# Kernel optimization log

Hardware: AMD Instinct MI355X
Metric: run time of the kernel (lower is better)

Reference implementation:

```python
import jax, jax.numpy as jnp
import numpy as np

N_HEADS = 4
TAU = 0.1

def _ln(x, w, b):
    m = jnp.mean(x, axis=-1, keepdims=True)
    v = jnp.mean(jnp.square(x - m), axis=-1, keepdims=True)
    return (x - m) / jnp.sqrt(v + 1e-6) * w + b

def _l2norm(x):
    # torch F.normalize(dim=1): x / max(||x||_2, 1e-12)
    n = jnp.linalg.norm(x, axis=1, keepdims=True)
    return x / jnp.maximum(n, 1e-12)

def _sincos_pe(T, dim):
    pos = jnp.arange(T, dtype=jnp.float32)[:, None]
    div = jnp.exp(jnp.arange(0, dim, 2, dtype=jnp.float32) * (-np.log(10000.0) / dim))
    ang = pos * div[None, :]
    # interleave: even indices sin, odd indices cos
    return jnp.stack([jnp.sin(ang), jnp.cos(ang)], axis=-1).reshape(T, dim)

def reference(x, p1_w, p1_b, pln1_w, pln1_b, p2_w, pln2_w, pln2_b,
              in_proj_w, in_proj_b, out_proj_w, out_proj_b,
              ln1_w, ln1_b, lin1_w, lin1_b, lin2_w, lin2_b, ln2_w, ln2_b, head_w):
    B, T, D = x.shape
    E = p2_w.shape[0]           # bottleneck_dim = 256
    H = N_HEADS
    hd = E // H
    # projector: Linear -> LN -> GELU -> Linear(no bias) -> LN
    h = jax.nn.gelu(_ln(x.reshape(B * T, D) @ p1_w.T + p1_b, pln1_w, pln1_b), approximate=False)
    h = _ln(h @ p2_w.T, pln2_w, pln2_b).reshape(B, T, E)
    h = h + _sincos_pe(T, E)[None]
    causal = jnp.tril(jnp.ones((T, T), dtype=bool))
    L = in_proj_w.shape[0]
    for i in range(L):  # post-norm TransformerEncoderLayer
        qkv = h @ in_proj_w[i].T + in_proj_b[i]        # [B,T,3E]
        q, k, v = jnp.split(qkv, 3, axis=-1)
        q = q.reshape(B, T, H, hd).transpose(0, 2, 1, 3)
        k = k.reshape(B, T, H, hd).transpose(0, 2, 1, 3)
        v = v.reshape(B, T, H, hd).transpose(0, 2, 1, 3)
        scores = jnp.einsum('bhtd,bhsd->bhts', q, k) / np.float32(np.sqrt(hd))
        scores = jnp.where(causal[None, None], scores, -jnp.inf)
        probs = jax.nn.softmax(scores, axis=-1)        # materialized attn probs (eager path)
        attn = jnp.einsum('bhts,bhsd->bhtd', probs, v).transpose(0, 2, 1, 3).reshape(B, T, E)
        attn = attn @ out_proj_w[i].T + out_proj_b[i]
        h = _ln(h + attn, ln1_w[i], ln1_b[i])
        ff = jax.nn.gelu(h @ lin1_w[i].T + lin1_b[i], approximate=False) @ lin2_w[i].T + lin2_b[i]
        h = _ln(h + ff, ln2_w[i], ln2_b[i])
    flat = _l2norm(h.reshape(B * T, E))
    wn = _l2norm(head_w)
    return (flat @ wn.T / TAU).reshape(B, T, -1)

def setup_inputs() -> dict:
    key = jax.random.key(0)
    ks = jax.random.split(key, 8)
    B, T, D, E, HID, CLS, L = 2048, 20, 2048, 256, 1024, 1000, 2
    s = 0.02
    def w(k, shape):
        return jax.random.normal(k, shape, jnp.float32) * s
    return {
        'x': jax.random.normal(ks[0], (B, T, D), jnp.float32),
        'p1_w': w(ks[1], (HID, D)), 'p1_b': jnp.zeros((HID,), jnp.float32),
        'pln1_w': jnp.ones((HID,), jnp.float32), 'pln1_b': jnp.zeros((HID,), jnp.float32),
        'p2_w': w(ks[2], (E, HID)),
        'pln2_w': jnp.ones((E,), jnp.float32), 'pln2_b': jnp.zeros((E,), jnp.float32),
        'in_proj_w': w(ks[3], (L, 3 * E, E)), 'in_proj_b': jnp.zeros((L, 3 * E), jnp.float32),
        'out_proj_w': w(ks[4], (L, E, E)), 'out_proj_b': jnp.zeros((L, E), jnp.float32),
        'ln1_w': jnp.ones((L, E), jnp.float32), 'ln1_b': jnp.zeros((L, E), jnp.float32),
        'lin1_w': w(ks[5], (L, 4 * E, E)), 'lin1_b': jnp.zeros((L, 4 * E), jnp.float32),
        'lin2_w': w(ks[6], (L, E, 4 * E)), 'lin2_b': jnp.zeros((L, E), jnp.float32),
        'ln2_w': jnp.ones((L, E), jnp.float32), 'ln2_b': jnp.zeros((L, E), jnp.float32),
        'head_w': w(ks[7], (CLS, E)),
    }
```

## Files before the change

kernel.cpp:

```cpp
#include <hip/hip_runtime.h>
#include <math.h>

#define CDIV(a,b) (((a)+(b)-1)/(b))

typedef unsigned short bfu;
typedef short   s16x8 __attribute__((ext_vector_type(8)));
typedef float   f32x4 __attribute__((ext_vector_type(4)));

#define GLOAD16(gp, lp) __builtin_amdgcn_global_load_lds( \
    (const __attribute__((address_space(1))) void*)(gp),  \
    (__attribute__((address_space(3))) void*)(lp), 16, 0, 0)

static __device__ __forceinline__ float gelu_exact(float x) {
    return 0.5f * x * (1.0f + erff(x * 0.7071067811865475f));
}
static __device__ __forceinline__ bfu f2bf(float x) {
    unsigned int u = __float_as_uint(x);
    unsigned int r = u + 0x7fffu + ((u >> 16) & 1u);
    return (bfu)(r >> 16);
}
static __device__ __forceinline__ float bf2f(bfu b) {
    return __uint_as_float(((unsigned int)b) << 16);
}

static __device__ __forceinline__ float block_sum_256(float v, float* sbuf) {
    #pragma unroll
    for (int off = 32; off; off >>= 1) v += __shfl_down(v, off, 64);
    const int lane = threadIdx.x & 63;
    const int wid  = threadIdx.x >> 6;
    __syncthreads();
    if (lane == 0) sbuf[wid] = v;
    __syncthreads();
    return sbuf[0] + sbuf[1] + sbuf[2] + sbuf[3];
}

__global__ __launch_bounds__(256)
void cvt_kernel(const float* __restrict__ in, bfu* __restrict__ out, int n4)
{
    int i = blockIdx.x * 256 + threadIdx.x;
    const int stride = gridDim.x * 256;
    for (; i < n4; i += stride) {
        float4 f = ((const float4*)in)[i];
        ushort4 o;
        o.x = f2bf(f.x); o.y = f2bf(f.y); o.z = f2bf(f.z); o.w = f2bf(f.w);
        ((ushort4*)out)[i] = o;
    }
}

__global__ __launch_bounds__(256)
void cvt6_kernel(const float* __restrict__ s0, const float* __restrict__ s1,
                 const float* __restrict__ s2, const float* __restrict__ s3,
                 const float* __restrict__ s4, const float* __restrict__ s5,
                 bfu* __restrict__ dst)
{
    const int c0 = 524288;
    const int c1 = c0 + 65536;
    const int c2 = c1 + 98304;
    const int c3 = c2 + 32768;
    const int c4 = c3 + 131072;
    const int c5 = c4 + 131072;
    int i = blockIdx.x * 256 + threadIdx.x;
    const int stride = gridDim.x * 256;
    for (; i < c5; i += stride) {
        const float* s; int base;
        if      (i < c0) { s = s0; base = 0;  }
        else if (i < c1) { s = s1; base = c0; }
        else if (i < c2) { s = s2; base = c1; }
        else if (i < c3) { s = s3; base = c2; }
        else if (i < c4) { s = s4; base = c3; }
        else             { s = s5; base = c4; }
        float4 f = ((const float4*)s)[i - base];
        ushort4 o;
        o.x = f2bf(f.x); o.y = f2bf(f.y); o.z = f2bf(f.z); o.w = f2bf(f.w);
        ((ushort4*)dst)[i] = o;
    }
}

template<bool GELU_EP, bool OUT_BF16>
__global__ __launch_bounds__(256)
void mfma_gemm(const bfu* __restrict__ A, const bfu* __restrict__ W,
               const float* __restrict__ bias, void* __restrict__ Cv,
               int M, int N, int K, float scale, int ntx)
{
    __shared__ bfu As[128 * 32];
    __shared__ bfu Ws[128 * 32];

    const int tid = threadIdx.x;
    const int nwg = gridDim.x;
    const int lid = (nwg & 7) ? (int)blockIdx.x
                              : ((int)blockIdx.x & 7) * (nwg >> 3) + ((int)blockIdx.x >> 3);
    const int row0 = (lid / ntx) * 128;
    const int col0 = (lid % ntx) * 128;

    const int lane = tid & 63;
    const int wave = tid >> 6;
    const int wm = (wave >> 1) * 64;
    const int wn = (wave & 1) * 64;
    const int fr = lane & 15;
    const int fk = (lane >> 4) * 8;

    const int lrow = lane >> 2;
    const int lk   = (lane & 3) * 8;
    const bfu* al0 = A + (size_t)(row0 + wave * 32 + lrow) * K + lk;
    const bfu* al1 = al0 + (size_t)16 * K;
    const bfu* wl0 = W + (size_t)(col0 + wave * 32 + lrow) * K + lk;
    const bfu* wl1 = wl0 + (size_t)16 * K;
    bfu* ad0 = &As[(wave * 2    ) * 512];
    bfu* ad1 = &As[(wave * 2 + 1) * 512];
    bfu* wd0 = &Ws[(wave * 2    ) * 512];
    bfu* wd1 = &Ws[(wave * 2 + 1) * 512];

    f32x4 acc[4][4];
    #pragma unroll
    for (int i = 0; i < 4; ++i)
        #pragma unroll
        for (int j = 0; j < 4; ++j) acc[i][j] = (f32x4)0.f;

    for (int k0 = 0; k0 < K; k0 += 32) {
        GLOAD16(al0 + k0, ad0);
        GLOAD16(al1 + k0, ad1);
        GLOAD16(wl0 + k0, wd0);
        GLOAD16(wl1 + k0, wd1);
        __syncthreads();

        s16x8 af[4], wf[4];
        #pragma unroll
        for (int i = 0; i < 4; ++i) af[i] = *(const s16x8*)&As[(wm + 16*i + fr) * 32 + fk];
        #pragma unroll
        for (int j = 0; j < 4; ++j) wf[j] = *(const s16x8*)&Ws[(wn + 16*j + fr) * 32 + fk];

        #pragma unroll
        for (int i = 0; i < 4; ++i)
            #pragma unroll
            for (int j = 0; j < 4; ++j)
                acc[i][j] = __builtin_amdgcn_mfma_f32_16x16x32_bf16(af[i], wf[j], acc[i][j], 0, 0, 0);
        __syncthreads();
    }

    #pragma unroll
    for (int i = 0; i < 4; ++i) {
        const int r = row0 + wm + 16 * i + (lane >> 4) * 4;
        #pragma unroll
        for (int j = 0; j < 4; ++j) {
            const int c = col0 + wn + 16 * j + fr;
            if (c < N) {
                const float bsum = bias ? bias[c] : 0.f;
                #pragma unroll
                for (int rr = 0; rr < 4; ++rr) {
                    float v = acc[i][j][rr] + bsum;
                    if (GELU_EP) v = gelu_exact(v);
                    v *= scale;
                    if (OUT_BF16) ((bfu*)Cv)[(size_t)(r + rr) * N + c] = f2bf(v);
                    else          ((float*)Cv)[(size_t)(r + rr) * N + c] = v;
                }
            }
        }
    }
}

template<int VPT, bool GELU_EP, bool ADD_PE, bool RES, bool IN_BF16>
__global__ __launch_bounds__(256)
void ln_kernel(const void* __restrict__ Xv, const float* __restrict__ R,
               const float* __restrict__ w, const float* __restrict__ b,
               float* __restrict__ Yf, bfu* __restrict__ Yb, int T)
{
    const int W = VPT * 256;
    __shared__ float sbuf[4];
    const int row = blockIdx.x;

    float v[VPT];
    if (IN_BF16) {
        const bfu* xr = (const bfu*)Xv + (size_t)row * W;
        if (VPT == 4) {
            ushort4 t4 = *(const ushort4*)(xr + threadIdx.x * 4);
            v[0] = bf2f(t4.x); v[1] = bf2f(t4.y); v[2] = bf2f(t4.z); v[3] = bf2f(t4.w);
        } else {
            v[0] = bf2f(xr[threadIdx.x]);
        }
    } else {
        const float* xr = (const float*)Xv + (size_t)row * W;
        if (VPT == 4) {
            float4 t4 = *(const float4*)(xr + threadIdx.x * 4);
            v[0] = t4.x; v[1] = t4.y; v[2] = t4.z; v[3] = t4.w;
        } else {
            v[0] = xr[threadIdx.x];
        }
    }
    if (RES) {
        #pragma unroll
        for (int j = 0; j < VPT; ++j)
            v[j] += R[(size_t)row * W + ((VPT == 4) ? threadIdx.x * 4 + j : (int)threadIdx.x)];
    }

    float s = 0.f;
    #pragma unroll
    for (int j = 0; j < VPT; ++j) s += v[j];
    const float mean = block_sum_256(s, sbuf) / (float)W;

    float q = 0.f;
    #pragma unroll
    for (int j = 0; j < VPT; ++j) { float d = v[j] - mean; q += d * d; }
    const float var  = block_sum_256(q, sbuf) / (float)W;
    const float rstd = rsqrtf(var + 1e-6f);

    #pragma unroll
    for (int j = 0; j < VPT; ++j) {
        const int c = (VPT == 4) ? (threadIdx.x * 4 + j) : (int)threadIdx.x;
        float y = (v[j] - mean) * rstd * w[c] + b[c];
        if (GELU_EP) y = gelu_exact(y);
        if (ADD_PE) {
            const int t = row % T;
            const float cc  = (float)(c & ~1);
            const float div = expf(cc * (-9.210340371976184f / 256.0f));
            const float ang = (float)t * div;
            y += (c & 1) ? cosf(ang) : sinf(ang);
        }
        if (Yf) Yf[(size_t)row * W + c] = y;
        if (Yb) Yb[(size_t)row * W + c] = f2bf(y);
    }
}

__global__ __launch_bounds__(64)
void attn_kernel(const bfu* __restrict__ qkv, bfu* __restrict__ out,
                 int B, int T, int H)
{
    __shared__ float qs[20][65];
    __shared__ float ks[20][65];
    __shared__ float vs[20][65];
    __shared__ float probs[64];

    const int blk = blockIdx.x;
    const int b = blk / H;
    const int h = blk % H;
    const int tid = threadIdx.x;

    for (int t = 0; t < T; ++t) {
        const bfu* base = qkv + (size_t)(b * T + t) * 768 + h * 64 + tid;
        qs[t][tid] = bf2f(base[0]);
        ks[t][tid] = bf2f(base[256]);
        vs[t][tid] = bf2f(base[512]);
    }
    __syncthreads();

    for (int t = 0; t < T; ++t) {
        float sc = -INFINITY;
        if (tid <= t) {
            float s = 0.f;
            #pragma unroll
            for (int d = 0; d < 64; ++d) s = fmaf(qs[t][d], ks[tid][d], s);
            sc = s * 0.125f;
        }
        float m = sc;
        #pragma unroll
        for (int off = 32; off; off >>= 1) m = fmaxf(m, __shfl_xor(m, off, 64));
        float p = (tid <= t) ? expf(sc - m) : 0.f;
        float sum = p;
        #pragma unroll
        for (int off = 32; off; off >>= 1) sum += __shfl_xor(sum, off, 64);
        p /= sum;
        probs[tid] = p;
        __syncthreads();

        float o = 0.f;
        for (int s = 0; s <= t; ++s) o = fmaf(probs[s], vs[s][tid], o);
        out[(size_t)(b * T + t) * 256 + h * 64 + tid] = f2bf(o);
        __syncthreads();
    }
}

__global__ __launch_bounds__(256)
void l2norm_kernel(const float* __restrict__ X, bfu* __restrict__ Y)
{
    __shared__ float sbuf[4];
    const int row = blockIdx.x;
    const float v = X[(size_t)row * 256 + threadIdx.x];
    float s = v * v;
    #pragma unroll
    for (int off = 32; off; off >>= 1) s += __shfl_down(s, off, 64);
    const int lane = threadIdx.x & 63, wid = threadIdx.x >> 6;
    if (lane == 0) sbuf[wid] = s;
    __syncthreads();
    float n = sqrtf(sbuf[0] + sbuf[1] + sbuf[2] + sbuf[3]);
    n = fmaxf(n, 1e-12f);
    Y[(size_t)row * 256 + threadIdx.x] = f2bf(v / n);
}

extern "C" void kernel_launch(void* const* d_in, const int* in_sizes, int n_in,
                              void* d_out, int out_size, void* d_ws, size_t ws_size,
                              hipStream_t stream)
{
    const float* x         = (const float*)d_in[0];
    const float* p1_w      = (const float*)d_in[1];
    const float* p1_b      = (const float*)d_in[2];
    const float* pln1_w    = (const float*)d_in[3];
    const float* pln1_b    = (const float*)d_in[4];
    const float* p2_w      = (const float*)d_in[5];
    const float* pln2_w    = (const float*)d_in[6];
    const float* pln2_b    = (const float*)d_in[7];
    const float* in_proj_w = (const float*)d_in[8];
    const float* in_proj_b = (const float*)d_in[9];
    const float* out_proj_w= (const float*)d_in[10];
    const float* out_proj_b= (const float*)d_in[11];
    const float* ln1_w     = (const float*)d_in[12];
    const float* ln1_b     = (const float*)d_in[13];
    const float* lin1_w    = (const float*)d_in[14];
    const float* lin1_b    = (const float*)d_in[15];
    const float* lin2_w    = (const float*)d_in[16];
    const float* lin2_b    = (const float*)d_in[17];
    const float* ln2_w     = (const float*)d_in[18];
    const float* ln2_b     = (const float*)d_in[19];
    const float* head_w    = (const float*)d_in[20];

    const int B = 2048, T = 20, E = 256, HID = 1024, CLS = 1000, L = 2, H = 4;
    const int M = B * T;
    const int D = 2048;

    char* p = (char*)d_ws;
    bfu*   xb     = (bfu*)p;    p += (size_t)M * D * 2;
    bfu*   h1b    = (bfu*)p;    p += (size_t)M * HID * 2;
    bfu*   wblk   = (bfu*)p;    p += (size_t)3932160 * 2;
    bfu*   wnb    = (bfu*)p;    p += (size_t)1024 * E * 2;

    char* q = (char*)xb;
    float* h      = (float*)q;  q += (size_t)M * E * 4;
    float* ffout  = (float*)q;  q += (size_t)M * E * 4;
    bfu*   hb     = (bfu*)q;    q += (size_t)M * E * 2;
    bfu*   abf    = (bfu*)q;    q += (size_t)M * E * 2;

    bfu* p1wb  = wblk;
    bfu* p2wb  = p1wb  + (size_t)HID * D;
    bfu* qkvwb = p2wb  + (size_t)E * HID;
    bfu* outwb = qkvwb + (size_t)L * 3 * E * E;
    bfu* l1wb  = outwb + (size_t)L * E * E;
    bfu* l2wb  = l1wb  + (size_t)L * 4 * E * E;

    float* out   = (float*)d_out;
    bfu*   qkvb  = (bfu*)d_out;
    float* attnp = (float*)d_out;

    cvt_kernel<<<2048, 256, 0, stream>>>(x, xb, M * D / 4);
    cvt6_kernel<<<2048, 256, 0, stream>>>(p1_w, p2_w, in_proj_w, out_proj_w, lin1_w, lin2_w, wblk);

    mfma_gemm<false, true><<<dim3(8 * (M/128)), 256, 0, stream>>>(
        xb, p1wb, p1_b, h1b, M, HID, D, 1.f, 8);
    ln_kernel<4, true, false, false, true><<<M, 256, 0, stream>>>(
        h1b, nullptr, pln1_w, pln1_b, nullptr, h1b, T);
    mfma_gemm<false, false><<<dim3(2 * (M/128)), 256, 0, stream>>>(
        h1b, p2wb, nullptr, h, M, E, HID, 1.f, 2);
    ln_kernel<1, false, true, false, false><<<M, 256, 0, stream>>>(
        h, nullptr, pln2_w, pln2_b, h, hb, T);

    for (int l = 0; l < L; ++l) {
        mfma_gemm<false, true><<<dim3(6 * (M/128)), 256, 0, stream>>>(
            hb, qkvwb + (size_t)l * 3*E*E, in_proj_b + (size_t)l * 3*E, qkvb, M, 3*E, E, 1.f, 6);
        attn_kernel<<<B * H, 64, 0, stream>>>(qkvb, abf, B, T, H);
        mfma_gemm<false, false><<<dim3(2 * (M/128)), 256, 0, stream>>>(
            abf, outwb + (size_t)l * E*E, out_proj_b + (size_t)l * E, attnp, M, E, E, 1.f, 2);
        ln_kernel<1, false, false, true, false><<<M, 256, 0, stream>>>(
            h, attnp, ln1_w + (size_t)l * E, ln1_b + (size_t)l * E, h, hb, T);
        mfma_gemm<true, true><<<dim3(8 * (M/128)), 256, 0, stream>>>(
            hb, l1wb + (size_t)l * 4*E*E, lin1_b + (size_t)l * 4*E, h1b, M, HID, E, 1.f, 8);
        mfma_gemm<false, false><<<dim3(2 * (M/128)), 256, 0, stream>>>(
            h1b, l2wb + (size_t)l * E*4*E, lin2_b + (size_t)l * E, ffout, M, E, HID, 1.f, 2);
        ln_kernel<1, false, false, true, false><<<M, 256, 0, stream>>>(
            h, ffout, ln2_w + (size_t)l * E, ln2_b + (size_t)l * E, h, hb, T);
    }

    l2norm_kernel<<<M, 256, 0, stream>>>(h, hb);
    l2norm_kernel<<<CLS, 256, 0, stream>>>(head_w, wnb);
    mfma_gemm<false, false><<<dim3(8 * (M/128)), 256, 0, stream>>>(
        hb, wnb, nullptr, out, M, CLS, E, 10.f, 8);
}
```

Measured before the change: 1.391 ms.

## Double-buffer GEMM LDS with XOR swizzle; wave-per-row LayerNorm and precomputed PE

The GEMM now double-buffers its LDS tiles. It prefetches the next K-slice with global_load_lds while running MFMAs on the current one, applies an XOR swizzle to cut LDS bank conflicts, and raises wave priority around the MFMA block. The 256-wide LayerNorm and L2-norm kernels now map one row per wave with float4 loads and shuffle-only reductions, which removes block-level syncs. A 1024-wide LN variant is specialised. The positional encoding is computed once into a small table instead of per element with transcendentals. Trade-offs are twice the LDS use, which may lower occupancy, and one extra tiny launch.

```diff
diff --git a/kernel.cpp b/kernel.cpp
--- a/kernel.cpp
+++ b/kernel.cpp
@@ -22,16 +22,10 @@
 static __device__ __forceinline__ float bf2f(bfu b) {
     return __uint_as_float(((unsigned int)b) << 16);
 }
-
-static __device__ __forceinline__ float block_sum_256(float v, float* sbuf) {
+static __device__ __forceinline__ float wave_sum(float v) {
     #pragma unroll
-    for (int off = 32; off; off >>= 1) v += __shfl_down(v, off, 64);
-    const int lane = threadIdx.x & 63;
-    const int wid  = threadIdx.x >> 6;
-    __syncthreads();
-    if (lane == 0) sbuf[wid] = v;
-    __syncthreads();
-    return sbuf[0] + sbuf[1] + sbuf[2] + sbuf[3];
+    for (int off = 32; off; off >>= 1) v += __shfl_xor(v, off, 64);
+    return v;
 }
 
 __global__ __launch_bounds__(256)
@@ -76,14 +70,24 @@
     }
 }
 
+__global__ __launch_bounds__(256)
+void pe_kernel(float* __restrict__ pe)
+{
+    const int t = blockIdx.x;
+    const int c = threadIdx.x;
+    const float div = expf((float)(c & ~1) * (-9.210340371976184f / 256.0f));
+    const float ang = (float)t * div;
+    pe[t * 256 + c] = (c & 1) ? cosf(ang) : sinf(ang);
+}
+
 template<bool GELU_EP, bool OUT_BF16>
 __global__ __launch_bounds__(256)
 void mfma_gemm(const bfu* __restrict__ A, const bfu* __restrict__ W,
                const float* __restrict__ bias, void* __restrict__ Cv,
                int M, int N, int K, float scale, int ntx)
 {
-    __shared__ bfu As[128 * 32];
-    __shared__ bfu Ws[128 * 32];
+    __shared__ bfu As[2][128 * 32];
+    __shared__ bfu Ws[2][128 * 32];
 
     const int tid = threadIdx.x;
     const int nwg = gridDim.x;
@@ -97,18 +101,16 @@
     const int wm = (wave >> 1) * 64;
     const int wn = (wave & 1) * 64;
     const int fr = lane & 15;
-    const int fk = (lane >> 4) * 8;
+    const int fs = (((lane >> 4) ^ (fr & 3))) * 8;
 
     const int lrow = lane >> 2;
-    const int lk   = (lane & 3) * 8;
+    const int lk   = (((lane & 3) ^ (lrow & 3))) * 8;
     const bfu* al0 = A + (size_t)(row0 + wave * 32 + lrow) * K + lk;
     const bfu* al1 = al0 + (size_t)16 * K;
     const bfu* wl0 = W + (size_t)(col0 + wave * 32 + lrow) * K + lk;
     const bfu* wl1 = wl0 + (size_t)16 * K;
-    bfu* ad0 = &As[(wave * 2    ) * 512];
-    bfu* ad1 = &As[(wave * 2 + 1) * 512];
-    bfu* wd0 = &Ws[(wave * 2    ) * 512];
-    bfu* wd1 = &Ws[(wave * 2 + 1) * 512];
+    const int ld0 = (wave * 2    ) * 512;
+    const int ld1 = (wave * 2 + 1) * 512;
 
     f32x4 acc[4][4];
     #pragma unroll
@@ -116,25 +118,42 @@
         #pragma unroll
         for (int j = 0; j < 4; ++j) acc[i][j] = (f32x4)0.f;
 
+    GLOAD16(al0, &As[0][ld0]);
+    GLOAD16(al1, &As[0][ld1]);
+    GLOAD16(wl0, &Ws[0][ld0]);
+    GLOAD16(wl1, &Ws[0][ld1]);
+    asm volatile("s_waitcnt vmcnt(0)" ::: "memory");
+    __builtin_amdgcn_s_barrier();
+
+    int cur = 0;
     for (int k0 = 0; k0 < K; k0 += 32) {
-        GLOAD16(al0 + k0, ad0);
-        GLOAD16(al1 + k0, ad1);
-        GLOAD16(wl0 + k0, wd0);
-        GLOAD16(wl1 + k0, wd1);
-        __syncthreads();
+        const bool more = (k0 + 32) < K;
+        if (more) {
+            GLOAD16(al0 + k0 + 32, &As[cur ^ 1][ld0]);
+            GLOAD16(al1 + k0 + 32, &As[cur ^ 1][ld1]);
+            GLOAD16(wl0 + k0 + 32, &Ws[cur ^ 1][ld0]);
+            GLOAD16(wl1 + k0 + 32, &Ws[cur ^ 1][ld1]);
+        }
 
         s16x8 af[4], wf[4];
         #pragma unroll
-        for (int i = 0; i < 4; ++i) af[i] = *(const s16x8*)&As[(wm + 16*i + fr) * 32 + fk];
-        #pragma unroll
-        for (int j = 0; j < 4; ++j) wf[j] = *(const s16x8*)&Ws[(wn + 16*j + fr) * 32 + fk];
-
+        for (int i = 0; i < 4; ++i) af[i] = *(const s16x8*)&As[cur][(wm + 16*i + fr) * 32 + fs];
+        #pragma unroll
+        for (int j = 0; j < 4; ++j) wf[j] = *(const s16x8*)&Ws[cur][(wn + 16*j + fr) * 32 + fs];
+
+        __builtin_amdgcn_s_setprio(1);
         #pragma unroll
         for (int i = 0; i < 4; ++i)
             #pragma unroll
             for (int j = 0; j < 4; ++j)
                 acc[i][j] = __builtin_amdgcn_mfma_f32_16x16x32_bf16(af[i], wf[j], acc[i][j], 0, 0, 0);
-        __syncthreads();
+        __builtin_amdgcn_s_setprio(0);
+
+        if (more) {
+            asm volatile("s_waitcnt vmcnt(0)" ::: "memory");
+            __builtin_amdgcn_s_barrier();
+        }
+        cur ^= 1;
     }
 
     #pragma unroll
@@ -158,65 +177,78 @@
     }
 }
 
-template<int VPT, bool GELU_EP, bool ADD_PE, bool RES, bool IN_BF16>
-__global__ __launch_bounds__(256)
-void ln_kernel(const void* __restrict__ Xv, const float* __restrict__ R,
-               const float* __restrict__ w, const float* __restrict__ b,
-               float* __restrict__ Yf, bfu* __restrict__ Yb, int T)
-{
-    const int W = VPT * 256;
+__global__ __launch_bounds__(256)
+void ln1024_kernel(const bfu* __restrict__ X, const float* __restrict__ w,
+                   const float* __restrict__ b, bfu* __restrict__ Y)
+{
     __shared__ float sbuf[4];
     const int row = blockIdx.x;
-
-    float v[VPT];
-    if (IN_BF16) {
-        const bfu* xr = (const bfu*)Xv + (size_t)row * W;
-        if (VPT == 4) {
-            ushort4 t4 = *(const ushort4*)(xr + threadIdx.x * 4);
-            v[0] = bf2f(t4.x); v[1] = bf2f(t4.y); v[2] = bf2f(t4.z); v[3] = bf2f(t4.w);
-        } else {
-            v[0] = bf2f(xr[threadIdx.x]);
-        }
-    } else {
-        const float* xr = (const float*)Xv + (size_t)row * W;
-        if (VPT == 4) {
-            float4 t4 = *(const float4*)(xr + threadIdx.x * 4);
-            v[0] = t4.x; v[1] = t4.y; v[2] = t4.z; v[3] = t4.w;
-        } else {
-            v[0] = xr[threadIdx.x];
-        }
-    }
-    if (RES) {
-        #pragma unroll
-        for (int j = 0; j < VPT; ++j)
-            v[j] += R[(size_t)row * W + ((VPT == 4) ? threadIdx.x * 4 + j : (int)threadIdx.x)];
-    }
-
-    float s = 0.f;
-    #pragma unroll
-    for (int j = 0; j < VPT; ++j) s += v[j];
-    const float mean = block_sum_256(s, sbuf) / (float)W;
+    const bfu* xr = X + (size_t)row * 1024;
+
+    ushort4 t4 = *(const ushort4*)(xr + threadIdx.x * 4);
+    float v[4] = {bf2f(t4.x), bf2f(t4.y), bf2f(t4.z), bf2f(t4.w)};
+
+    float s = v[0] + v[1] + v[2] + v[3];
+    s = wave_sum(s);
+    const int lane = threadIdx.x & 63, wid = threadIdx.x >> 6;
+    if (lane == 0) sbuf[wid] = s;
+    __syncthreads();
+    const float mean = (sbuf[0] + sbuf[1] + sbuf[2] + sbuf[3]) * (1.f / 1024.f);
 
     float q = 0.f;
     #pragma unroll
-    for (int j = 0; j < VPT; ++j) { float d = v[j] - mean; q += d * d; }
-    const float var  = block_sum_256(q, sbuf) / (float)W;
+    for (int j = 0; j < 4; ++j) { float d = v[j] - mean; q += d * d; }
+    q = wave_sum(q);
+    __syncthreads();
+    if (lane == 0) sbuf[wid] = q;
+    __syncthreads();
+    const float var  = (sbuf[0] + sbuf[1] + sbuf[2] + sbuf[3]) * (1.f / 1024.f);
     const float rstd = rsqrtf(var + 1e-6f);
 
+    ushort4 o;
     #pragma unroll
-    for (int j = 0; j < VPT; ++j) {
-        const int c = (VPT == 4) ? (threadIdx.x * 4 + j) : (int)threadIdx.x;
-        float y = (v[j] - mean) * rstd * w[c] + b[c];
-        if (GELU_EP) y = gelu_exact(y);
-        if (ADD_PE) {
-            const int t = row % T;
-            const float cc  = (float)(c & ~1);
-            const float div = expf(cc * (-9.210340371976184f / 256.0f));
-            const float ang = (float)t * div;
-            y += (c & 1) ? cosf(ang) : sinf(ang);
-        }
-        if (Yf) Yf[(size_t)row * W + c] = y;
-        if (Yb) Yb[(size_t)row * W + c] = f2bf(y);
+    for (int j = 0; j < 4; ++j) {
+        const int c = threadIdx.x * 4 + j;
+        float y = gelu_exact((v[j] - mean) * rstd * w[c] + b[c]);
+        ((bfu*)&o)[j] = f2bf(y);
+    }
+    *(ushort4*)(Y + (size_t)row * 1024 + threadIdx.x * 4) = o;
+}
+
+template<bool ADD_PE, bool RES>
+__global__ __launch_bounds__(256)
+void ln256_kernel(const float* __restrict__ X, const float* __restrict__ R,
+                  const float* __restrict__ w, const float* __restrict__ b,
+                  const float* __restrict__ pe, float* __restrict__ Yf,
+                  bfu* __restrict__ Yb, int T)
+{
+    const int row  = blockIdx.x * 4 + (threadIdx.x >> 6);
+    const int lane = threadIdx.x & 63;
+
+    float4 v = *(const float4*)(X + (size_t)row * 256 + lane * 4);
+    if (RES) {
+        float4 r4 = *(const float4*)(R + (size_t)row * 256 + lane * 4);
+        v.x += r4.x; v.y += r4.y; v.z += r4.z; v.w += r4.w;
+    }
+
+    const float mean = wave_sum(v.x + v.y + v.z + v.w) * (1.f / 256.f);
+    float q = (v.x-mean)*(v.x-mean) + (v.y-mean)*(v.y-mean)
+            + (v.z-mean)*(v.z-mean) + (v.w-mean)*(v.w-mean);
+    const float rstd = rsqrtf(wave_sum(q) * (1.f / 256.f) + 1e-6f);
+
+    const float4 w4 = *(const float4*)(w + lane * 4);
+    const float4 b4 = *(const float4*)(b + lane * 4);
+    float y[4] = {(v.x-mean)*rstd*w4.x + b4.x, (v.y-mean)*rstd*w4.y + b4.y,
+                  (v.z-mean)*rstd*w4.z + b4.z, (v.w-mean)*rstd*w4.w + b4.w};
+    if (ADD_PE) {
+        const float4 p4 = *(const float4*)(pe + (size_t)(row % T) * 256 + lane * 4);
+        y[0] += p4.x; y[1] += p4.y; y[2] += p4.z; y[3] += p4.w;
+    }
+
+    if (Yf) *(float4*)(Yf + (size_t)row * 256 + lane * 4) = float4{y[0], y[1], y[2], y[3]};
+    if (Yb) {
+        ushort4 o = {f2bf(y[0]), f2bf(y[1]), f2bf(y[2]), f2bf(y[3])};
+        *(ushort4*)(Yb + (size_t)row * 256 + lane * 4) = o;
     }
 }
 
@@ -271,18 +303,13 @@
 __global__ __launch_bounds__(256)
 void l2norm_kernel(const float* __restrict__ X, bfu* __restrict__ Y)
 {
-    __shared__ float sbuf[4];
-    const int row = blockIdx.x;
-    const float v = X[(size_t)row * 256 + threadIdx.x];
-    float s = v * v;
-    #pragma unroll
-    for (int off = 32; off; off >>= 1) s += __shfl_down(s, off, 64);
-    const int lane = threadIdx.x & 63, wid = threadIdx.x >> 6;
-    if (lane == 0) sbuf[wid] = s;
-    __syncthreads();
-    float n = sqrtf(sbuf[0] + sbuf[1] + sbuf[2] + sbuf[3]);
-    n = fmaxf(n, 1e-12f);
-    Y[(size_t)row * 256 + threadIdx.x] = f2bf(v / n);
+    const int row  = blockIdx.x * 4 + (threadIdx.x >> 6);
+    const int lane = threadIdx.x & 63;
+    float4 v = *(const float4*)(X + (size_t)row * 256 + lane * 4);
+    float n = sqrtf(wave_sum(v.x*v.x + v.y*v.y + v.z*v.z + v.w*v.w));
+    n = 1.f / fmaxf(n, 1e-12f);
+    ushort4 o = {f2bf(v.x*n), f2bf(v.y*n), f2bf(v.z*n), f2bf(v.w*n)};
+    *(ushort4*)(Y + (size_t)row * 256 + lane * 4) = o;
 }
 
 extern "C" void kernel_launch(void* const* d_in, const int* in_sizes, int n_in,
@@ -320,6 +347,7 @@
     bfu*   h1b    = (bfu*)p;    p += (size_t)M * HID * 2;
     bfu*   wblk   = (bfu*)p;    p += (size_t)3932160 * 2;
     bfu*   wnb    = (bfu*)p;    p += (size_t)1024 * E * 2;
+    float* pe     = (float*)p;  p += (size_t)T * 256 * 4;
 
     char* q = (char*)xb;
     float* h      = (float*)q;  q += (size_t)M * E * 4;
@@ -340,15 +368,15 @@
 
     cvt_kernel<<<2048, 256, 0, stream>>>(x, xb, M * D / 4);
     cvt6_kernel<<<2048, 256, 0, stream>>>(p1_w, p2_w, in_proj_w, out_proj_w, lin1_w, lin2_w, wblk);
+    pe_kernel<<<T, 256, 0, stream>>>(pe);
 
     mfma_gemm<false, true><<<dim3(8 * (M/128)), 256, 0, stream>>>(
         xb, p1wb, p1_b, h1b, M, HID, D, 1.f, 8);
-    ln_kernel<4, true, false, false, true><<<M, 256, 0, stream>>>(
-        h1b, nullptr, pln1_w, pln1_b, nullptr, h1b, T);
+    ln1024_kernel<<<M, 256, 0, stream>>>(h1b, pln1_w, pln1_b, h1b);
     mfma_gemm<false, false><<<dim3(2 * (M/128)), 256, 0, stream>>>(
         h1b, p2wb, nullptr, h, M, E, HID, 1.f, 2);
-    ln_kernel<1, false, true, false, false><<<M, 256, 0, stream>>>(
-        h, nullptr, pln2_w, pln2_b, h, hb, T);
+    ln256_kernel<true, false><<<M/4, 256, 0, stream>>>(
+        h, nullptr, pln2_w, pln2_b, pe, h, hb, T);
 
     for (int l = 0; l < L; ++l) {
         mfma_gemm<false, true><<<dim3(6 * (M/128)), 256, 0, stream>>>(
@@ -356,18 +384,18 @@
         attn_kernel<<<B * H, 64, 0, stream>>>(qkvb, abf, B, T, H);
         mfma_gemm<false, false><<<dim3(2 * (M/128)), 256, 0, stream>>>(
             abf, outwb + (size_t)l * E*E, out_proj_b + (size_t)l * E, attnp, M, E, E, 1.f, 2);
-        ln_kernel<1, false, false, true, false><<<M, 256, 0, stream>>>(
-            h, attnp, ln1_w + (size_t)l * E, ln1_b + (size_t)l * E, h, hb, T);
+        ln256_kernel<false, true><<<M/4, 256, 0, stream>>>(
+            h, attnp, ln1_w + (size_t)l * E, ln1_b + (size_t)l * E, nullptr, h, hb, T);
         mfma_gemm<true, true><<<dim3(8 * (M/128)), 256, 0, stream>>>(
             hb, l1wb + (size_t)l * 4*E*E, lin1_b + (size_t)l * 4*E, h1b, M, HID, E, 1.f, 8);
         mfma_gemm<false, false><<<dim3(2 * (M/128)), 256, 0, stream>>>(
             h1b, l2wb + (size_t)l * E*4*E, lin2_b + (size_t)l * E, ffout, M, E, HID, 1.f, 2);
-        ln_kernel<1, false, false, true, false><<<M, 256, 0, stream>>>(
-            h, ffout, ln2_w + (size_t)l * E, ln2_b + (size_t)l * E, h, hb, T);
-    }
-
-    l2norm_kernel<<<M, 256, 0, stream>>>(h, hb);
-    l2norm_kernel<<<CLS, 256, 0, stream>>>(head_w, wnb);
+        ln256_kernel<false, true><<<M/4, 256, 0, stream>>>(
+            h, ffout, ln2_w + (size_t)l * E, ln2_b + (size_t)l * E, nullptr, h, hb, T);
+    }
+
+    l2norm_kernel<<<M/4, 256, 0, stream>>>(h, hb);
+    l2norm_kernel<<<CLS/4, 256, 0, stream>>>(head_w, wnb);
     mfma_gemm<false, false><<<dim3(8 * (M/128)), 256, 0, stream>>>(
         hb, wnb, nullptr, out, M, CLS, E, 10.f, 8);
 }
```

New measurement: 1.556 ms. +11.8%, slower.
